# Performance work log

Hardware: AMD Instinct MI355X
Metric: run time of the kernel (lower is better)

## Reference

```python
import jax, jax.numpy as jnp
import numpy as np

D_MODEL = 128; N_HEADS = 8; N_LEVELS = 1; N_POINTS = 8
MAX_RES = 10.0
B, H_SP, W_SP = 8, 64, 64


def setup_inputs() -> dict:
    key = jax.random.key(0)
    ks = jax.random.split(key, 8)
    s = 0.02
    f32 = jnp.float32
    return {
        "nbr_fea": jax.random.normal(ks[0], (B, D_MODEL, H_SP, W_SP), f32),
        "ext_fea": jax.random.normal(ks[1], (B, D_MODEL, H_SP, W_SP), f32),
        "W_val": jax.random.normal(ks[2], (D_MODEL, D_MODEL), f32) * s,
        "b_val": jnp.zeros((D_MODEL,), f32),
        "W_off": jax.random.normal(ks[3], (D_MODEL, N_HEADS * N_LEVELS * N_POINTS * 2), f32) * s,
        "b_off": jax.random.normal(ks[4], (N_HEADS * N_LEVELS * N_POINTS * 2,), f32) * s,
        "W_attn": jax.random.normal(ks[5], (D_MODEL, N_HEADS * N_LEVELS * N_POINTS), f32) * s,
        "b_attn": jnp.zeros((N_HEADS * N_LEVELS * N_POINTS,), f32),
        "W_out": jax.random.normal(ks[6], (D_MODEL, D_MODEL), f32) * s,
        "b_out": jnp.zeros((D_MODEL,), f32),
    }


def _deform_attn_align(nbr_fea, ext_fea, W_val, b_val, W_off, b_off, W_attn, b_attn, W_out, b_out):
    b, c, h, w = nbr_fea.shape
    L = h * w
    dh = c // N_HEADS
    # flatten b c h w -> b (h w) c
    query = jnp.transpose(ext_fea, (0, 2, 3, 1)).reshape(b, L, c)
    vin = jnp.transpose(nbr_fea, (0, 2, 3, 1)).reshape(b, L, c)

    # value projection (mask is all-False -> no masked fill needed)
    value = (vin @ W_val + b_val).reshape(b, L, N_HEADS, dh)
    vh = jnp.transpose(value, (0, 2, 1, 3))  # [b, H, L, dh]

    # sampling offsets, clamped by max_residue_magnitude * tanh
    off = MAX_RES * jnp.tanh(query @ W_off + b_off)
    off = off.reshape(b, L, N_HEADS, N_POINTS, 2)  # single level
    attn = jax.nn.softmax((query @ W_attn + b_attn).reshape(b, L, N_HEADS, N_POINTS), axis=-1)

    # reference points in [0,1]; valid_ratio == 1 since padding mask is all-False
    yy, xx = jnp.meshgrid(jnp.arange(h, dtype=jnp.float32), jnp.arange(w, dtype=jnp.float32), indexing="ij")
    ref = jnp.stack([(xx.reshape(-1) + 0.5) / w, (yy.reshape(-1) + 0.5) / h], axis=-1)  # [L, 2]
    norm = jnp.array([w, h], jnp.float32)  # offset_normalizer [W, H]
    loc = ref[None, :, None, None, :] + off / norm  # [b, L, H, P, 2]

    # grid_sample(align_corners=False, padding_mode='zeros') pixel coordinates
    px = jnp.transpose(loc[..., 0] * w - 0.5, (0, 2, 1, 3))  # [b, H, L, P]
    py = jnp.transpose(loc[..., 1] * h - 0.5, (0, 2, 1, 3))

    x0 = jnp.floor(px); y0 = jnp.floor(py)
    fx = px - x0; fy = py - y0
    x0i = x0.astype(jnp.int32); y0i = y0.astype(jnp.int32)

    def gather(xi, yi):
        valid = (xi >= 0) & (xi < w) & (yi >= 0) & (yi < h)
        idx = jnp.clip(yi, 0, h - 1) * w + jnp.clip(xi, 0, w - 1)  # [b, H, L, P]
        g = jnp.take_along_axis(vh, idx.reshape(b, N_HEADS, L * N_POINTS)[..., None], axis=2)
        return g.reshape(b, N_HEADS, L, N_POINTS, dh) * valid[..., None]

    samp = (gather(x0i, y0i) * ((1.0 - fx) * (1.0 - fy))[..., None]
            + gather(x0i + 1, y0i) * (fx * (1.0 - fy))[..., None]
            + gather(x0i, y0i + 1) * ((1.0 - fx) * fy)[..., None]
            + gather(x0i + 1, y0i + 1) * (fx * fy)[..., None])  # [b, H, L, P, dh]

    aw = jnp.transpose(attn, (0, 2, 1, 3))  # [b, H, L, P]
    out = jnp.sum(samp * aw[..., None], axis=3)  # [b, H, L, dh]
    out = jnp.transpose(out, (0, 2, 1, 3)).reshape(b, L, c)
    out = out @ W_out + b_out
    return jnp.transpose(out.reshape(b, h, w, c), (0, 3, 1, 2))  # b c h w


def reference(nbr_fea, ext_fea, W_val, b_val, W_off, b_off, W_attn, b_attn, W_out, b_out):
    return _deform_attn_align(nbr_fea, ext_fea, W_val, b_val, W_off, b_off, W_attn, b_attn, W_out, b_out)
```

## Files before the change

### kernel.cpp

```cpp
#include <hip/hip_runtime.h>
#include <cstdint>

#define HB 8
#define CM 128
#define NHEAD 8
#define NPT 8
#define DHD 16
#define HS 64
#define WS 64
#define LTOT 4096
#define NQA 192
#define QAP 196
#define LFP 132

typedef float floatx4 __attribute__((ext_vector_type(4)));
typedef short bf16x8 __attribute__((ext_vector_type(8)));

__device__ __forceinline__ unsigned short f2bf_rne(float x) {
  unsigned u = __float_as_uint(x);
  return (unsigned short)((u + 0x7FFFu + ((u >> 16) & 1)) >> 16);
}
__device__ __forceinline__ void split_bf(float x, unsigned short& h, unsigned short& l) {
  unsigned u = __float_as_uint(x);
  h = (unsigned short)(u >> 16);
  float r = x - __uint_as_float(u & 0xFFFF0000u);
  l = (unsigned short)(__float_as_uint(r) >> 16);
}
__device__ __forceinline__ float fast_tanh(float x) {
  float e = __expf(2.0f * x);
  return 1.0f - 2.0f / (e + 1.0f);
}
__device__ __forceinline__ void bf8_fma(floatx4& oa, floatx4& ob, const uint4 r, const float wc) {
  floatx4 va = {__uint_as_float(r.x << 16), __uint_as_float(r.x & 0xFFFF0000u),
                __uint_as_float(r.y << 16), __uint_as_float(r.y & 0xFFFF0000u)};
  floatx4 vb = {__uint_as_float(r.z << 16), __uint_as_float(r.z & 0xFFFF0000u),
                __uint_as_float(r.w << 16), __uint_as_float(r.w & 0xFFFF0000u)};
  oa += va * wc;
  ob += vb * wc;
}

__global__ __launch_bounds__(256) void prep(const float* __restrict__ Wv,
                                            const float* __restrict__ Wo,
                                            const float* __restrict__ Wa,
                                            const float* __restrict__ Ww,
                                            const float* __restrict__ bo,
                                            const float* __restrict__ ba,
                                            unsigned short* __restrict__ wf_val,
                                            unsigned short* __restrict__ wf_qa,
                                            unsigned short* __restrict__ wf_out,
                                            float* __restrict__ bias_qa) {
  const int gid = blockIdx.x * 256 + threadIdx.x;
  const int k4 = gid / 448;
  const int ng = gid - k4 * 448;

  const float* src;
  unsigned short* dst;
  int Nsrc, Nn, nd, n;
  if (ng < 128) {        src = Wv; dst = wf_val; Nsrc = 128; Nn = 128; n = ng;        nd = n; }
  else if (ng < 256) {   src = Wo; dst = wf_qa;  Nsrc = 128; Nn = 192; n = ng - 128;  nd = n; }
  else if (ng < 320) {   src = Wa; dst = wf_qa;  Nsrc = 64;  Nn = 192; n = ng - 256;  nd = n + 128; }
  else {                 src = Ww; dst = wf_out; Nsrc = 128; Nn = 128; n = ng - 320;  nd = n; }

  ushort4 hi, lo;
  split_bf(src[(k4 * 4 + 0) * Nsrc + n], hi.x, lo.x);
  split_bf(src[(k4 * 4 + 1) * Nsrc + n], hi.y, lo.y);
  split_bf(src[(k4 * 4 + 2) * Nsrc + n], hi.z, lo.z);
  split_bf(src[(k4 * 4 + 3) * Nsrc + n], hi.w, lo.w);
  const int off = (k4 >> 1) * Nn * 8 + nd * 8 + (k4 & 1) * 4;
  *(ushort4*)(dst + off) = hi;
  *(ushort4*)(dst + Nn * 128 + off) = lo;

  if (gid < 128) bias_qa[gid] = bo[gid];
  else if (gid < 192) bias_qa[gid] = ba[gid - 128];
}

__global__ __launch_bounds__(256, 4) void gemm_val(const float* __restrict__ nbr,
                                                   const unsigned short* __restrict__ WF,
                                                   const float* __restrict__ bias,
                                                   unsigned short* __restrict__ value) {
  __shared__ __align__(16) char smem[33792];
  unsigned short* AB = (unsigned short*)smem;
  const int t = threadIdx.x;
  const int ml0 = blockIdx.x * 64;
  const int b = blockIdx.y;

  {
    const float* src = nbr + (size_t)b * CM * LTOT + ml0;
    const int x = t & 63, kq = t >> 6;
#pragma unroll
    for (int i = 0; i < 8; i++) {
      const int kb = kq * 4 + i * 16;
      ushort4 hi, lo;
      split_bf(src[(size_t)(kb + 0) * LTOT + x], hi.x, lo.x);
      split_bf(src[(size_t)(kb + 1) * LTOT + x], hi.y, lo.y);
      split_bf(src[(size_t)(kb + 2) * LTOT + x], hi.z, lo.z);
      split_bf(src[(size_t)(kb + 3) * LTOT + x], hi.w, lo.w);
      const int off = x * 128 + (((kb >> 3) ^ (x & 15)) << 3) + (kb & 7);
      *(ushort4*)(AB + off) = hi;
      *(ushort4*)(AB + 8192 + off) = lo;
    }
  }
  __syncthreads();

  const int w = t >> 6, lane = t & 63;
  const int wm = (w >> 1) * 32, wn = (w & 1) * 64;
  const int nl = lane & 15, q = lane >> 4;

  floatx4 acc[2][4];
#pragma unroll
  for (int mt = 0; mt < 2; mt++)
#pragma unroll
    for (int j = 0; j < 4; j++) acc[mt][j] = {0.0f, 0.0f, 0.0f, 0.0f};

#pragma unroll
  for (int K0 = 0; K0 < 4; K0++) {
    bf16x8 ah[2], al[2];
#pragma unroll
    for (int mt = 0; mt < 2; mt++) {
      const int m = wm + mt * 16 + nl;
      const int off = m * 128 + (((K0 * 4 + q) ^ (m & 15)) << 3);
      ah[mt] = *(bf16x8*)(AB + off);
      al[mt] = *(bf16x8*)(AB + 8192 + off);
    }
#pragma unroll
    for (int j = 0; j < 4; j++) {
      const size_t o = (size_t)(K0 * 4 + q) * CM * 8 + (wn + j * 16 + nl) * 8;
      const bf16x8 wh = *(const bf16x8*)(WF + o);
      const bf16x8 wl = *(const bf16x8*)(WF + (size_t)CM * 128 + o);
#pragma unroll
      for (int mt = 0; mt < 2; mt++) {
        acc[mt][j] = __builtin_amdgcn_mfma_f32_16x16x32_bf16(al[mt], wh, acc[mt][j], 0, 0, 0);
        acc[mt][j] = __builtin_amdgcn_mfma_f32_16x16x32_bf16(ah[mt], wl, acc[mt][j], 0, 0, 0);
        acc[mt][j] = __builtin_amdgcn_mfma_f32_16x16x32_bf16(ah[mt], wh, acc[mt][j], 0, 0, 0);
      }
    }
  }

  __syncthreads();
  float* LF = (float*)smem;
#pragma unroll
  for (int j = 0; j < 4; j++) {
    const int gc = wn + j * 16 + nl;
    const float bv = bias[gc];
#pragma unroll
    for (int mt = 0; mt < 2; mt++)
#pragma unroll
      for (int r = 0; r < 4; r++)
        LF[(wm + mt * 16 + q * 4 + r) * LFP + gc] = acc[mt][j][r] + bv;
  }
  __syncthreads();
#pragma unroll
  for (int i = 0; i < 4; i++) {
    const int c = t + i * 256;
    const int h = c >> 7, rem = c & 127, l = rem >> 1, half = rem & 1;
    const float* sp = LF + l * LFP + h * 16 + half * 8;
    uint4 st;
    st.x = ((unsigned)f2bf_rne(sp[1]) << 16) | f2bf_rne(sp[0]);
    st.y = ((unsigned)f2bf_rne(sp[3]) << 16) | f2bf_rne(sp[2]);
    st.z = ((unsigned)f2bf_rne(sp[5]) << 16) | f2bf_rne(sp[4]);
    st.w = ((unsigned)f2bf_rne(sp[7]) << 16) | f2bf_rne(sp[6]);
    *(uint4*)(value + ((size_t)(b * NHEAD + h) * LTOT + ml0 + l) * DHD + half * 8) = st;
  }
}

__global__ __launch_bounds__(256, 2) void samp(const float* __restrict__ ext,
                                               const unsigned short* __restrict__ value,
                                               const unsigned short* __restrict__ wf_qa,
                                               const unsigned short* __restrict__ wf_out,
                                               const float* __restrict__ bias_qa,
                                               const float* __restrict__ b_out,
                                               float* __restrict__ out) {
  __shared__ __align__(16) char smem[25088];
  unsigned short* AB = (unsigned short*)smem;
  float* qaT = (float*)smem;
  unsigned short* FR = (unsigned short*)smem;

  const int t = threadIdx.x;
  const int b = blockIdx.x & 7;
  const int ml0 = (blockIdx.x >> 3) * 32;
  const int w = t >> 6, lane = t & 63;
  const int nl = lane & 15, q = lane >> 4;

  {
    const float* src = ext + (size_t)b * CM * LTOT + ml0;
    const int x = t & 31, kq = t >> 5;
#pragma unroll
    for (int i = 0; i < 4; i++) {
      const int kb = i * 32 + kq * 4;
      ushort4 hi, lo;
      split_bf(src[(size_t)(kb + 0) * LTOT + x], hi.x, lo.x);
      split_bf(src[(size_t)(kb + 1) * LTOT + x], hi.y, lo.y);
      split_bf(src[(size_t)(kb + 2) * LTOT + x], hi.z, lo.z);
      split_bf(src[(size_t)(kb + 3) * LTOT + x], hi.w, lo.w);
      const int off = x * 128 + (((kb >> 3) ^ (x & 15)) << 3) + (kb & 7);
      *(ushort4*)(AB + off) = hi;
      *(ushort4*)(AB + 4096 + off) = lo;
    }
  }
  __syncthreads();

  {
    const int wm = (w & 1) * 16;
    const int wn = (w >> 1) * 96;
    floatx4 acc[6];
#pragma unroll
    for (int j = 0; j < 6; j++) acc[j] = {0.0f, 0.0f, 0.0f, 0.0f};
#pragma unroll
    for (int K0 = 0; K0 < 4; K0++) {
      const int m = wm + nl;
      const int off = m * 128 + (((K0 * 4 + q) ^ (m & 15)) << 3);
      const bf16x8 ah = *(bf16x8*)(AB + off);
      const bf16x8 al = *(bf16x8*)(AB + 4096 + off);
#pragma unroll
      for (int j = 0; j < 6; j++) {
        const size_t o = (size_t)(K0 * 4 + q) * NQA * 8 + (wn + j * 16 + nl) * 8;
        const bf16x8 wh = *(const bf16x8*)(wf_qa + o);
        const bf16x8 wl = *(const bf16x8*)(wf_qa + (size_t)NQA * 128 + o);
        acc[j] = __builtin_amdgcn_mfma_f32_16x16x32_bf16(al, wh, acc[j], 0, 0, 0);
        acc[j] = __builtin_amdgcn_mfma_f32_16x16x32_bf16(ah, wl, acc[j], 0, 0, 0);
        acc[j] = __builtin_amdgcn_mfma_f32_16x16x32_bf16(ah, wh, acc[j], 0, 0, 0);
      }
    }
    __syncthreads();
#pragma unroll
    for (int j = 0; j < 6; j++) {
      const int n = wn + j * 16 + nl;
      const float bv = bias_qa[n];
#pragma unroll
      for (int r = 0; r < 4; r++)
        qaT[(wm + q * 4 + r) * QAP + n] = acc[j][r] + bv;
    }
  }
  __syncthreads();

  float px[8], py[8], aw[8];
  const int ll = t >> 3, h = t & 7;
  {
    const float* qrow = qaT + ll * QAP;
    float4 of[4];
#pragma unroll
    for (int j = 0; j < 4; j++) of[j] = *(const float4*)(qrow + h * 16 + j * 4);
    const float4 lga = *(const float4*)(qrow + 128 + h * 8);
    const float4 lgb = *(const float4*)(qrow + 128 + h * 8 + 4);
    const float lg[8] = {lga.x, lga.y, lga.z, lga.w, lgb.x, lgb.y, lgb.z, lgb.w};
    float m = lg[0];
#pragma unroll
    for (int p = 1; p < 8; p++) m = fmaxf(m, lg[p]);
    float e[8], s = 0.0f;
#pragma unroll
    for (int p = 0; p < 8; p++) { e[p] = __expf(lg[p] - m); s += e[p]; }
    const float inv = 1.0f / s;
    const int l = ml0 + ll;
    const float xf = (float)(l & (WS - 1));
    const float yf = (float)(l >> 6);
#pragma unroll
    for (int p = 0; p < 8; p++) {
      const float ox = (p & 1) ? of[p >> 1].z : of[p >> 1].x;
      const float oy = (p & 1) ? of[p >> 1].w : of[p >> 1].y;
      px[p] = xf + 10.0f * fast_tanh(ox);
      py[p] = yf + 10.0f * fast_tanh(oy);
      aw[p] = e[p] * inv;
    }
  }
  __syncthreads();

  {
    const unsigned hb = (unsigned)(b * NHEAD + h) * LTOT * DHD;
    const int llm = ll & 15;
#pragma unroll
    for (int hf = 0; hf < 2; hf++) {
      floatx4 oa = {0.f, 0.f, 0.f, 0.f}, ob = oa;
#pragma unroll
      for (int p = 0; p < 8; p++) {
        const float x0f = floorf(px[p]), y0f = floorf(py[p]);
        const float fx = px[p] - x0f, fy = py[p] - y0f;
        const int ix = (int)x0f, iy = (int)y0f;
        const float a = aw[p];
        float wc[4];
        unsigned adr[4];
#pragma unroll
        for (int c = 0; c < 4; c++) {
          const int cdx = c & 1, cdy = c >> 1;
          const int jx = ix + cdx, jy = iy + cdy;
          const float wx = cdx ? fx : 1.0f - fx;
          const float wy = cdy ? fy : 1.0f - fy;
          const bool valid = ((unsigned)jx < WS) & ((unsigned)jy < HS);
          wc[c] = valid ? a * wx * wy : 0.0f;
          const int cx = min(max(jx, 0), WS - 1);
          const int cy = min(max(jy, 0), HS - 1);
          adr[c] = hb + (unsigned)((cy << 6) + cx) * DHD + hf * 8;
        }
        uint4 r[4];
#pragma unroll
        for (int c = 0; c < 4; c++) r[c] = *(const uint4*)(value + adr[c]);
#pragma unroll
        for (int c = 0; c < 4; c++) bf8_fma(oa, ob, r[c], wc[c]);
      }
      const int off = ll * 128 + (((h * 2 + hf) ^ llm) << 3);
      uint4 st;
      st.x = ((unsigned)f2bf_rne(oa[1]) << 16) | f2bf_rne(oa[0]);
      st.y = ((unsigned)f2bf_rne(oa[3]) << 16) | f2bf_rne(oa[2]);
      st.z = ((unsigned)f2bf_rne(ob[1]) << 16) | f2bf_rne(ob[0]);
      st.w = ((unsigned)f2bf_rne(ob[3]) << 16) | f2bf_rne(ob[2]);
      *(uint4*)(FR + off) = st;
    }
  }
  __syncthreads();

  {
    const int wm = (w & 1) * 16;
    const int wn = (w >> 1) * 64;
    floatx4 acc[4];
#pragma unroll
    for (int j = 0; j < 4; j++) acc[j] = {0.0f, 0.0f, 0.0f, 0.0f};
#pragma unroll
    for (int K0 = 0; K0 < 4; K0++) {
      const int m = wm + nl;
      const int off = m * 128 + (((K0 * 4 + q) ^ (m & 15)) << 3);
      const bf16x8 ah = *(bf16x8*)(FR + off);
#pragma unroll
      for (int j = 0; j < 4; j++) {
        const int n = wn + j * 16 + nl;
        const size_t o = (size_t)(K0 * 4 + q) * CM * 8 + n * 8;
        const bf16x8 wh = *(const bf16x8*)(wf_out + o);
        const bf16x8 wl = *(const bf16x8*)(wf_out + (size_t)CM * 128 + o);
        acc[j] = __builtin_amdgcn_mfma_f32_16x16x32_bf16(ah, wl, acc[j], 0, 0, 0);
        acc[j] = __builtin_amdgcn_mfma_f32_16x16x32_bf16(ah, wh, acc[j], 0, 0, 0);
      }
    }
#pragma unroll
    for (int j = 0; j < 4; j++) {
      const int gc = wn + j * 16 + nl;
      const float bv = b_out[gc];
      float4 st = {acc[j][0] + bv, acc[j][1] + bv, acc[j][2] + bv, acc[j][3] + bv};
      *(float4*)(out + ((size_t)b * CM + gc) * LTOT + ml0 + wm + q * 4) = st;
    }
  }
}

extern "C" void kernel_launch(void* const* d_in, const int* in_sizes, int n_in,
                              void* d_out, int out_size, void* d_ws, size_t ws_size,
                              hipStream_t stream) {
  const float* nbr    = (const float*)d_in[0];
  const float* ext    = (const float*)d_in[1];
  const float* W_val  = (const float*)d_in[2];
  const float* b_val  = (const float*)d_in[3];
  const float* W_off  = (const float*)d_in[4];
  const float* b_off  = (const float*)d_in[5];
  const float* W_attn = (const float*)d_in[6];
  const float* b_attn = (const float*)d_in[7];
  const float* W_out  = (const float*)d_in[8];
  const float* b_out  = (const float*)d_in[9];
  float* out = (float*)d_out;

  unsigned short* value = (unsigned short*)d_ws;
  unsigned short* wf_val = value + (size_t)HB * NHEAD * LTOT * DHD;
  unsigned short* wf_qa  = wf_val + 128 * 128 * 2;
  unsigned short* wf_out = wf_qa + 192 * 128 * 2;
  float* bias_qa = (float*)(wf_out + 128 * 128 * 2);

  prep<<<56, 256, 0, stream>>>(W_val, W_off, W_attn, W_out, b_off, b_attn,
                               wf_val, wf_qa, wf_out, bias_qa);
  gemm_val<<<dim3(64, HB), 256, 0, stream>>>(nbr, wf_val, b_val, value);
  samp<<<dim3(128 * HB), 256, 0, stream>>>(ext, value, wf_qa, wf_out, bias_qa, b_out, out);
}
```

Before: 150.4 us.

## Pack horizontally adjacent value pixels so bilinear taps load contiguously

Adds a qpack kernel that rewrites the bf16 value tensor so each pixel stores its own 16 channels interleaved with those of its right neighbour (x+1, clamped). The sampling kernel then fetches each bilinear row pair with one contiguous 32-byte read per row instead of four scattered 16-byte gathers. Corner weights are rebuilt with clamped base coordinates and tent functions to handle the borders. This costs an extra kernel launch plus a doubled-size copy of the value tensor written and read through memory, and it changes how out-of-range corners are masked.

```diff
diff --git a/kernel.cpp b/kernel.cpp
--- a/kernel.cpp
+++ b/kernel.cpp
@@ -163,8 +163,29 @@
   }
 }
 
+__global__ __launch_bounds__(256) void qpack(const unsigned short* __restrict__ value,
+                                             unsigned short* __restrict__ p2) {
+  const int b = blockIdx.x & 7;
+  const int chunk = blockIdx.x >> 3;
+  const int h = chunk >> 4;
+  const int y = (chunk & 15) * 4 + (threadIdx.x >> 6);
+  const int x = threadIdx.x & 63;
+  const int bh = b * NHEAD + h;
+  const unsigned short* vb = value + (size_t)bh * LTOT * DHD;
+  const int xp = min(x + 1, WS - 1);
+  const uint4* s0 = (const uint4*)(vb + (y * WS + x) * DHD);
+  const uint4* s1 = (const uint4*)(vb + (y * WS + xp) * DHD);
+  const uint4 c0h0 = s0[0], c0h1 = s0[1];
+  const uint4 c1h0 = s1[0], c1h1 = s1[1];
+  uint4* d = (uint4*)(p2 + ((size_t)bh * LTOT + y * WS + x) * 32);
+  d[0] = c0h0;
+  d[1] = c1h0;
+  d[2] = c0h1;
+  d[3] = c1h1;
+}
+
 __global__ __launch_bounds__(256, 2) void samp(const float* __restrict__ ext,
-                                               const unsigned short* __restrict__ value,
+                                               const unsigned short* __restrict__ p2,
                                                const unsigned short* __restrict__ wf_qa,
                                                const unsigned short* __restrict__ wf_out,
                                                const float* __restrict__ bias_qa,
@@ -265,7 +286,7 @@
   __syncthreads();
 
   {
-    const unsigned hb = (unsigned)(b * NHEAD + h) * LTOT * DHD;
+    const size_t pb = (size_t)(b * NHEAD + h) * LTOT * 32;
     const int llm = ll & 15;
 #pragma unroll
     for (int hf = 0; hf < 2; hf++) {
@@ -273,28 +294,28 @@
 #pragma unroll
       for (int p = 0; p < 8; p++) {
         const float x0f = floorf(px[p]), y0f = floorf(py[p]);
-        const float fx = px[p] - x0f, fy = py[p] - y0f;
-        const int ix = (int)x0f, iy = (int)y0f;
+        const int qx = min(max((int)x0f, 0), WS - 1);
+        const int qy = min(max((int)y0f, 0), HS - 1);
+        const float tx = px[p] - (float)qx;
+        const float ty = py[p] - (float)qy;
+        const float hx0 = fmaxf(0.0f, 1.0f - fabsf(tx));
+        float hx1 = fmaxf(0.0f, 1.0f - fabsf(tx - 1.0f));
+        const float hy0 = fmaxf(0.0f, 1.0f - fabsf(ty));
+        float hy1 = fmaxf(0.0f, 1.0f - fabsf(ty - 1.0f));
+        if (qx + 1 >= WS) hx1 = 0.0f;
+        if (qy + 1 >= HS) hy1 = 0.0f;
         const float a = aw[p];
-        float wc[4];
-        unsigned adr[4];
-#pragma unroll
-        for (int c = 0; c < 4; c++) {
-          const int cdx = c & 1, cdy = c >> 1;
-          const int jx = ix + cdx, jy = iy + cdy;
-          const float wx = cdx ? fx : 1.0f - fx;
-          const float wy = cdy ? fy : 1.0f - fy;
-          const bool valid = ((unsigned)jx < WS) & ((unsigned)jy < HS);
-          wc[c] = valid ? a * wx * wy : 0.0f;
-          const int cx = min(max(jx, 0), WS - 1);
-          const int cy = min(max(jy, 0), HS - 1);
-          adr[c] = hb + (unsigned)((cy << 6) + cx) * DHD + hf * 8;
-        }
-        uint4 r[4];
-#pragma unroll
-        for (int c = 0; c < 4; c++) r[c] = *(const uint4*)(value + adr[c]);
-#pragma unroll
-        for (int c = 0; c < 4; c++) bf8_fma(oa, ob, r[c], wc[c]);
+        const float ay0 = a * hy0, ay1 = a * hy1;
+        const unsigned r0 = (unsigned)(qy * WS + qx) * 32 + hf * 16;
+        const unsigned r1 = (unsigned)(min(qy + 1, HS - 1) * WS + qx) * 32 + hf * 16;
+        const uint4* a0 = (const uint4*)(p2 + pb + r0);
+        const uint4* a1 = (const uint4*)(p2 + pb + r1);
+        const uint4 v00 = a0[0], v01 = a0[1];
+        const uint4 v10 = a1[0], v11 = a1[1];
+        bf8_fma(oa, ob, v00, ay0 * hx0);
+        bf8_fma(oa, ob, v01, ay0 * hx1);
+        bf8_fma(oa, ob, v10, ay1 * hx0);
+        bf8_fma(oa, ob, v11, ay1 * hx1);
       }
       const int off = ll * 128 + (((h * 2 + hf) ^ llm) << 3);
       uint4 st;
@@ -354,7 +375,8 @@
   float* out = (float*)d_out;
 
   unsigned short* value = (unsigned short*)d_ws;
-  unsigned short* wf_val = value + (size_t)HB * NHEAD * LTOT * DHD;
+  unsigned short* p2    = value + (size_t)HB * NHEAD * LTOT * DHD;
+  unsigned short* wf_val = p2 + (size_t)HB * NHEAD * LTOT * 32;
   unsigned short* wf_qa  = wf_val + 128 * 128 * 2;
   unsigned short* wf_out = wf_qa + 192 * 128 * 2;
   float* bias_qa = (float*)(wf_out + 128 * 128 * 2);
@@ -362,5 +384,6 @@
   prep<<<56, 256, 0, stream>>>(W_val, W_off, W_attn, W_out, b_off, b_attn,
                                wf_val, wf_qa, wf_out, bias_qa);
   gemm_val<<<dim3(64, HB), 256, 0, stream>>>(nbr, wf_val, b_val, value);
-  samp<<<dim3(128 * HB), 256, 0, stream>>>(ext, value, wf_qa, wf_out, bias_qa, b_out, out);
-}
+  qpack<<<1024, 256, 0, stream>>>(value, p2);
+  samp<<<dim3(128 * HB), 256, 0, stream>>>(ext, p2, wf_qa, wf_out, bias_qa, b_out, out);
+}
```

Result: slower. 161.5 us (+7.4%).

## Remap sampling threads so each wave handles one head across queries

Applied to the files above, without the earlier changes.

Sampling positions and attention weights are now written to shared memory, laid out per head/point, and the gather phase is reassigned. Each wave now processes one head for all 32 queries, with lane pairs covering the two 8-channel halves, instead of each thread handling one query-head over both halves. This is meant to make the value-gather addresses within a wave fall in a single head's value plane and to spread the gather work differently. The cost is extra shared memory (larger LDS footprint, which may lower occupancy) and additional LDS reads per point.

```diff
diff --git a/kernel.cpp b/kernel.cpp
--- a/kernel.cpp
+++ b/kernel.cpp
@@ -12,6 +12,7 @@
 #define NQA 192
 #define QAP 196
 #define LFP 132
+#define WPP 33
 
 typedef float floatx4 __attribute__((ext_vector_type(4)));
 typedef short bf16x8 __attribute__((ext_vector_type(8)));
@@ -170,10 +171,12 @@
                                                const float* __restrict__ bias_qa,
                                                const float* __restrict__ b_out,
                                                float* __restrict__ out) {
-  __shared__ __align__(16) char smem[25088];
+  __shared__ __align__(16) char smem[33792];
   unsigned short* AB = (unsigned short*)smem;
   float* qaT = (float*)smem;
-  unsigned short* FR = (unsigned short*)smem;
+  float2* WXY = (float2*)smem;
+  float* WA = (float*)(smem + 16896);
+  unsigned short* FR = (unsigned short*)(smem + 25344);
 
   const int t = threadIdx.x;
   const int b = blockIdx.x & 7;
@@ -233,15 +236,15 @@
   }
   __syncthreads();
 
-  float px[8], py[8], aw[8];
-  const int ll = t >> 3, h = t & 7;
-  {
+  {
+    const int ll = t >> 3, h = t & 7;
     const float* qrow = qaT + ll * QAP;
     float4 of[4];
 #pragma unroll
     for (int j = 0; j < 4; j++) of[j] = *(const float4*)(qrow + h * 16 + j * 4);
     const float4 lga = *(const float4*)(qrow + 128 + h * 8);
     const float4 lgb = *(const float4*)(qrow + 128 + h * 8 + 4);
+    __syncthreads();
     const float lg[8] = {lga.x, lga.y, lga.z, lga.w, lgb.x, lgb.y, lgb.z, lgb.w};
     float m = lg[0];
 #pragma unroll
@@ -257,25 +260,27 @@
     for (int p = 0; p < 8; p++) {
       const float ox = (p & 1) ? of[p >> 1].z : of[p >> 1].x;
       const float oy = (p & 1) ? of[p >> 1].w : of[p >> 1].y;
-      px[p] = xf + 10.0f * fast_tanh(ox);
-      py[p] = yf + 10.0f * fast_tanh(oy);
-      aw[p] = e[p] * inv;
-    }
-  }
-  __syncthreads();
-
-  {
-    const unsigned hb = (unsigned)(b * NHEAD + h) * LTOT * DHD;
-    const int llm = ll & 15;
-#pragma unroll
-    for (int hf = 0; hf < 2; hf++) {
+      WXY[(h * 8 + p) * WPP + ll] = {xf + 10.0f * fast_tanh(ox), yf + 10.0f * fast_tanh(oy)};
+      WA[(h * 8 + p) * WPP + ll] = e[p] * inv;
+    }
+  }
+  __syncthreads();
+
+  {
+    const int llq = lane >> 1, half = lane & 1;
+    const int llm = llq & 15;
+#pragma unroll
+    for (int hi2 = 0; hi2 < 2; hi2++) {
+      const int hh = w + hi2 * 4;
+      const unsigned short* vb = value + (size_t)(b * NHEAD + hh) * LTOT * DHD + half * 8;
       floatx4 oa = {0.f, 0.f, 0.f, 0.f}, ob = oa;
 #pragma unroll
       for (int p = 0; p < 8; p++) {
-        const float x0f = floorf(px[p]), y0f = floorf(py[p]);
-        const float fx = px[p] - x0f, fy = py[p] - y0f;
+        const float2 pxy = WXY[(hh * 8 + p) * WPP + llq];
+        const float a = WA[(hh * 8 + p) * WPP + llq];
+        const float x0f = floorf(pxy.x), y0f = floorf(pxy.y);
+        const float fx = pxy.x - x0f, fy = pxy.y - y0f;
         const int ix = (int)x0f, iy = (int)y0f;
-        const float a = aw[p];
         float wc[4];
         unsigned adr[4];
 #pragma unroll
@@ -288,15 +293,15 @@
           wc[c] = valid ? a * wx * wy : 0.0f;
           const int cx = min(max(jx, 0), WS - 1);
           const int cy = min(max(jy, 0), HS - 1);
-          adr[c] = hb + (unsigned)((cy << 6) + cx) * DHD + hf * 8;
+          adr[c] = (unsigned)((cy << 6) + cx) * DHD;
         }
         uint4 r[4];
 #pragma unroll
-        for (int c = 0; c < 4; c++) r[c] = *(const uint4*)(value + adr[c]);
+        for (int c = 0; c < 4; c++) r[c] = *(const uint4*)(vb + adr[c]);
 #pragma unroll
         for (int c = 0; c < 4; c++) bf8_fma(oa, ob, r[c], wc[c]);
       }
-      const int off = ll * 128 + (((h * 2 + hf) ^ llm) << 3);
+      const int off = llq * 128 + (((hh * 2 + half) ^ llm) << 3);
       uint4 st;
       st.x = ((unsigned)f2bf_rne(oa[1]) << 16) | f2bf_rne(oa[0]);
       st.y = ((unsigned)f2bf_rne(oa[3]) << 16) | f2bf_rne(oa[2]);
```

After: 136.6 us. -9.2%, faster.
